# Kernel optimization log

Measured on AMD Instinct MI355X. Metric: run time of the kernel, lower is better.

## Reference

```python
import jax, jax.numpy as jnp
import numpy as np
from jax.scipy.special import logsumexp

UNK_ID = 1
B, T, V = 128, 33, 25000
E, H, D = 256, 256, 512
N, C = 8192, 16384
L = T - 1


def setup_inputs() -> dict:
    key = jax.random.key(0)
    ks = jax.random.split(key, 12)
    input_memories = jax.random.normal(ks[0], (N, D), jnp.float32)
    # each target owns a contiguous block of N//B memories (every segment non-empty)
    origin = jnp.repeat(jnp.arange(B, dtype=jnp.int32), N // B)
    initial_states = jax.random.normal(ks[1], (B, H), jnp.float32)
    target_token_ids = jax.random.randint(ks[2], (B, T), 0, V)
    # copyable elements: pick (memory n, time l); flat idx into [N,L] and [B,L]
    mem_pick = jax.random.randint(ks[3], (C,), 0, N)
    t_pick = jax.random.randint(ks[4], (C,), 0, L)
    copyable_elements_idxs = mem_pick * L + t_pick
    copyable_elements_sample_idxs = origin[mem_pick] * L + t_pick
    target_lengths = jax.random.randint(ks[5], (B,), 1, L + 1)
    emb_weight = 0.02 * jax.random.normal(ks[6], (V, E), jnp.float32)
    gru_w_ih = 0.05 * jax.random.normal(ks[7], (3 * H, E), jnp.float32)
    gru_w_hh = 0.05 * jax.random.normal(ks[8], (3 * H, H), jnp.float32)
    gru_b_ih = jnp.zeros((3 * H,), jnp.float32)
    gru_b_hh = jnp.zeros((3 * H,), jnp.float32)
    w_std_att = 0.05 * jax.random.normal(ks[9], (H, D), jnp.float32)
    w_copy_att = 0.05 * jax.random.normal(ks[10], (H, D), jnp.float32)
    hidden_to_vocab = 0.01 * jax.random.normal(ks[11], (2 * H, E), jnp.float32)
    vocab_bias = jnp.zeros((V,), jnp.float32)
    return dict(input_memories=input_memories, input_memories_origin_idx=origin,
                initial_states=initial_states, target_token_ids=target_token_ids,
                copyable_elements_idxs=copyable_elements_idxs,
                copyable_elements_sample_idxs=copyable_elements_sample_idxs,
                target_lengths=target_lengths, emb_weight=emb_weight,
                gru_w_ih=gru_w_ih, gru_w_hh=gru_w_hh, gru_b_ih=gru_b_ih,
                gru_b_hh=gru_b_hh, w_std_att=w_std_att, w_copy_att=w_copy_att,
                hidden_to_vocab=hidden_to_vocab, vocab_bias=vocab_bias)


def _gru(x, h0, w_ih, w_hh, b_ih, b_hh):
    # x: [B,L,E], h0: [B,H] -> outputs [B,L,H], last state [B,H]
    def step(h, xt):
        gi = xt @ w_ih.T + b_ih
        gh = h @ w_hh.T + b_hh
        ir, iz, inew = jnp.split(gi, 3, axis=-1)
        hr, hz, hnew = jnp.split(gh, 3, axis=-1)
        r = jax.nn.sigmoid(ir + hr)
        z = jax.nn.sigmoid(iz + hz)
        n = jnp.tanh(inew + r * hnew)
        h_next = (1.0 - z) * n + z * h
        return h_next, h_next
    h_last, ys = jax.lax.scan(step, h0, jnp.swapaxes(x, 0, 1))
    return jnp.swapaxes(ys, 0, 1), h_last


def _seg_log_softmax(x, idx, num_seg):
    m = jax.ops.segment_max(x, idx, num_segments=num_seg)
    x_sh = x - m[idx]
    s = jax.ops.segment_sum(jnp.exp(x_sh), idx, num_segments=num_seg)
    return x_sh - jnp.log(s)[idx]


def _seg_logsumexp(x, idx, num_seg):
    m = jax.ops.segment_max(x, idx, num_segments=num_seg)
    m_safe = jnp.where(jnp.isfinite(m), m, 0.0)
    s = jax.ops.segment_sum(jnp.exp(x - m_safe[idx]), idx, num_segments=num_seg)
    return jnp.where(s > 0, jnp.log(jnp.where(s > 0, s, 1.0)) + m_safe, -jnp.inf)


def reference(input_memories, input_memories_origin_idx, initial_states,
              target_token_ids, copyable_elements_idxs,
              copyable_elements_sample_idxs, target_lengths, emb_weight,
              gru_w_ih, gru_w_hh, gru_b_ih, gru_b_hh, w_std_att, w_copy_att,
              hidden_to_vocab, vocab_bias):
    origin = input_memories_origin_idx
    b, t = target_token_ids.shape
    l = t - 1
    tok_in = target_token_ids[:, :-1]
    tok_out = target_token_ids[:, 1:]

    x = emb_weight[tok_in]                                   # [B,L,E]
    out_states, _ = _gru(x, initial_states, gru_w_ih, gru_w_hh, gru_b_ih, gru_b_hh)
    std_reps = input_memories @ w_std_att.T                  # [N,H]
    copy_reps = input_memories @ w_copy_att.T                # [N,H]
    out_per_input = out_states[origin]                       # [N,L,H]
    std_scores = jnp.einsum('nlh,nh->nl', out_per_input, std_reps)
    copy_scores = jnp.einsum('nlh,nh->nl', out_per_input, copy_reps)

    std_logprobs = _seg_log_softmax(std_scores, origin, b)   # [N,L]
    std_mul = jnp.exp(std_logprobs)[:, :, None] * std_reps[:, None, :]
    std_out = jax.ops.segment_sum(std_mul, origin, num_segments=b)  # [B,L,H]

    cat = jnp.concatenate([std_out, out_states], axis=-1)    # [B,L,2H]
    target_scores = (cat @ hidden_to_vocab) @ emb_weight.T + vocab_bias  # [B,L,V]

    total_copy = _seg_logsumexp(copy_scores, origin, b)      # [B,L]
    all_scores = jnp.concatenate([target_scores, total_copy[:, :, None]], axis=-1)
    norm = logsumexp(all_scores, axis=-1)                    # [B,L]
    target_logprobs = target_scores - norm[:, :, None]
    copy_logprobs = copy_scores - norm[origin]               # [N,L]

    num_valid = jax.ops.segment_sum(jnp.ones_like(copyable_elements_sample_idxs),
                                    copyable_elements_sample_idxs,
                                    num_segments=b * l)
    valid_copy = num_valid.reshape(b, l) > 0
    unk_loc = tok_out == UNK_ID
    mask = valid_copy & unk_loc

    gen_lp = jnp.take_along_axis(target_logprobs, tok_out[:, :, None], axis=-1)[..., 0]
    gen_lp = jnp.where(mask, -jnp.inf, gen_lp)

    cc = _seg_logsumexp(copy_logprobs.reshape(-1)[copyable_elements_idxs],
                        copyable_elements_sample_idxs, b * l).reshape(b, l)

    any_lp = logsumexp(jnp.stack([gen_lp, cc]), axis=0)      # [B,L]
    len_mask = (jnp.arange(l)[None, :] < target_lengths[:, None]).astype(jnp.float32)
    per_seq = (any_lp * len_mask).sum(-1) / len_mask.sum(-1)
    return -per_seq.mean()
```

## Files before the change

### kernel.cpp

```cpp
#include <hip/hip_runtime.h>
#include <hip/hip_bf16.h>

#define UNK 1
constexpr int B  = 128, T = 33, V = 25000, E = 256, H = 256, D = 512;
constexpr int N  = 8192, C = 16384, L = 32;
constexpr int BL = B * L;
constexpr int VP = 25088;

typedef __attribute__((ext_vector_type(8))) short bf16x8;
typedef __attribute__((ext_vector_type(4))) float fx4;
typedef unsigned short u16;
typedef unsigned int u32;

__device__ __forceinline__ u16 f2b(float f) {
  u32 u = __float_as_uint(f);
  u += 0x7FFFu + ((u >> 16) & 1u);
  return (u16)(u >> 16);
}
__device__ __forceinline__ float b2f(u16 s) { return __uint_as_float(((u32)s) << 16); }
__device__ __forceinline__ float fsigm(float x) { return 1.f / (1.f + __expf(-x)); }
__device__ __forceinline__ float ftanh(float x) {
  float cx = fminf(fmaxf(x, -15.f), 15.f);
  float e = __expf(2.f * cx);
  return (e - 1.f) / (e + 1.f);
}
__device__ __forceinline__ u32 fkey(float f) {
  u32 b = __float_as_uint(f);
  return (b & 0x80000000u) ? ~b : (b | 0x80000000u);
}
__device__ __forceinline__ float fdec(u32 k) {
  u32 b = (k & 0x80000000u) ? (k & 0x7FFFFFFFu) : ~k;
  return __uint_as_float(b);
}
__device__ __forceinline__ void lcomb(float& M, float& S, float m2, float s2) {
  float Mn = fmaxf(M, m2);
  float a = (S  > 0.f) ? S  * expf(M  - Mn) : 0.f;
  float b = (s2 > 0.f) ? s2 * expf(m2 - Mn) : 0.f;
  M = Mn; S = a + b;
}
__device__ __forceinline__ void gload16(const void* g, void* l) {
  __builtin_amdgcn_global_load_lds(
      (const __attribute__((address_space(1))) void*)g,
      (__attribute__((address_space(3))) void*)l, 16, 0, 0);
}

constexpr int PB_EMB = VP * E / 1024;
constexpr int PB_MEM = N * D / 1024;
constexpr int PB_WIH = 768 * 256 / 1024;
constexpr int PB_WHH = 192;
constexpr int PB_WS  = 512 * 256 / 1024;
constexpr int PB_WC  = 128;
constexpr int PB_TR  = 512;
constexpr int PB_INIT= 16;
constexpr int PB_TOT = PB_EMB + PB_MEM + PB_WIH + PB_WHH + PB_WS + PB_WC + PB_TR + PB_INIT;

__device__ __forceinline__ void cvt4_at(const float* in, u16* out, int i) {
  float4 v = *(const float4*)&in[i];
  u16 r[4] = { f2b(v.x), f2b(v.y), f2b(v.z), f2b(v.w) };
  *(ushort4*)&out[i] = *(ushort4*)r;
}

__global__ void k_prep(const float* __restrict__ emb, const float* __restrict__ mem,
                       const float* __restrict__ wih, const float* __restrict__ whh,
                       const float* __restrict__ wstd, const float* __restrict__ wcpy,
                       const float* __restrict__ h2v,
                       u16* __restrict__ embb, u16* __restrict__ memb,
                       u16* __restrict__ wihb, u16* __restrict__ whb,
                       u16* __restrict__ wsb, u16* __restrict__ wcb,
                       u16* __restrict__ h2vtb,
                       u32* __restrict__ segk, float* __restrict__ segs,
                       int* __restrict__ nval, float* __restrict__ lacc) {
  int b = blockIdx.x, t = threadIdx.x;
  if (b < PB_EMB) {
    int i = (b * 256 + t) * 4;
    if (i + 3 < V * E) cvt4_at(emb, embb, i);
    else for (int j = 0; j < 4; ++j) embb[i + j] = (i + j < V * E) ? f2b(emb[i + j]) : (u16)0;
    return;
  }
  b -= PB_EMB;
  if (b < PB_MEM) { cvt4_at(mem, memb, (b * 256 + t) * 4); return; }
  b -= PB_MEM;
  if (b < PB_WIH) { cvt4_at(wih, wihb, (b * 256 + t) * 4); return; }
  b -= PB_WIH;
  if (b < PB_WHH) { cvt4_at(whh, whb, (b * 256 + t) * 4); return; }
  b -= PB_WHH;
  if (b < PB_WS)  { cvt4_at(wstd, wsb, (b * 256 + t) * 4); return; }
  b -= PB_WS;
  if (b < PB_WC)  { cvt4_at(wcpy, wcb, (b * 256 + t) * 4); return; }
  b -= PB_WC;
  if (b < PB_TR) {
    int f = b * 256 + t, j = f >> 9, k = f & 511;
    h2vtb[f] = f2b(h2v[k * 256 + j]);
    return;
  }
  b -= PB_TR;
  {
    int i = b * 256 + t;
    if (i < BL) { segk[i] = 0x007FFFFFu; segs[i] = 0.f; nval[i] = 0; }
    if (i == 0) lacc[0] = 0.f;
  }
}

__global__ __launch_bounds__(256, 2) void k_embgiM(const int* __restrict__ tok,
    const u16* __restrict__ eb, const u16* __restrict__ wih,
    const float* __restrict__ bih, const float* __restrict__ bhh,
    float* __restrict__ Git) {
  __shared__ __align__(16) u16 As[2][128 * 64];
  __shared__ __align__(16) u16 Bs2[2][128 * 64];
  int t = threadIdx.x;
  int m0 = blockIdx.x * 128, n0 = blockIdx.y * 128;
  int lane = t & 63, w = t >> 6, wm = w >> 1, wn = w & 1;
  int r16 = lane & 15, hi = lane >> 4;
  char* AsB = (char*)&As[0][0];
  char* BsB = (char*)&Bs2[0][0];
  int tk4[4];
#pragma unroll
  for (int i = 0; i < 4; ++i) {
    int row = (w * 4 + i) * 8 + (lane >> 3);
    int bl = m0 + row;
    tk4[i] = tok[(bl >> 5) * 33 + (bl & 31)];
  }
  fx4 acc[4][4] = {};
  auto stage = [&](int kt, int buf) {
#pragma unroll
    for (int i = 0; i < 4; ++i) {
      int s = (w * 4 + i) * 64 + lane;
      int row = s >> 3, sw = s & 7, c = sw ^ (row & 7);
      gload16(&eb[tk4[i] * 256 + kt * 64 + c * 8], AsB + buf * 16384 + (w * 4 + i) * 1024);
      gload16(&wih[(n0 + row) * 256 + kt * 64 + c * 8], BsB + buf * 16384 + (w * 4 + i) * 1024);
    }
  };
  stage(0, 0);
  for (int kt = 0; kt < 4; ++kt) {
    __syncthreads();
    if (kt < 3) stage(kt + 1, (kt + 1) & 1);
    int buf = kt & 1;
    bf16x8 afr[4][2], bfr[4][2];
#pragma unroll
    for (int mi = 0; mi < 4; ++mi)
#pragma unroll
      for (int kk = 0; kk < 2; ++kk) {
        int row = wm * 64 + mi * 16 + r16, cc = kk * 4 + hi;
        afr[mi][kk] = *(const bf16x8*)(AsB + buf * 16384 + (row * 8 + (cc ^ (row & 7))) * 16);
      }
#pragma unroll
    for (int ni = 0; ni < 4; ++ni)
#pragma unroll
      for (int kk = 0; kk < 2; ++kk) {
        int row = wn * 64 + ni * 16 + r16, cc = kk * 4 + hi;
        bfr[ni][kk] = *(const bf16x8*)(BsB + buf * 16384 + (row * 8 + (cc ^ (row & 7))) * 16);
      }
#pragma unroll
    for (int kk = 0; kk < 2; ++kk)
#pragma unroll
      for (int mi = 0; mi < 4; ++mi)
#pragma unroll
        for (int ni = 0; ni < 4; ++ni)
          acc[mi][ni] = __builtin_amdgcn_mfma_f32_16x16x32_bf16(afr[mi][kk], bfr[ni][kk], acc[mi][ni], 0, 0, 0);
  }
  float bihv[4];
#pragma unroll
  for (int ni = 0; ni < 4; ++ni) {
    int j = n0 + wn * 64 + ni * 16 + r16;
    bihv[ni] = bih[j] + (j < 512 ? bhh[j] : 0.f);
  }
#pragma unroll
  for (int mi = 0; mi < 4; ++mi)
#pragma unroll
    for (int ni = 0; ni < 4; ++ni)
#pragma unroll
      for (int q = 0; q < 4; ++q) {
        int bl = m0 + wm * 64 + mi * 16 + hi * 4 + q;
        int b = bl >> 5, st = bl & 31;
        int j  = n0 + wn * 64 + ni * 16 + r16;
        Git[(((b >> 4) * 32 + st) * 768 + j) * 16 + (b & 15)] = acc[mi][ni][q] + bihv[ni];
      }
}

__global__ __launch_bounds__(512, 2) void k_gru6(
    const float* __restrict__ Git, const u16* __restrict__ whb,
    const float* __restrict__ bhh, const float* __restrict__ h0,
    u16* __restrict__ outsb) {
  __shared__ u16 nfr[8 * 16 * 512];
  __shared__ u16 hbf[2][16 * 256];
  const int t = threadIdx.x;
  const int w = t >> 6, l = t & 63;
  const int lj = l & 15, lk = l >> 4;
  const int b0 = blockIdx.x * 16;

  bf16x8 fr[2][8], fz[2][8];
#pragma unroll
  for (int jh = 0; jh < 2; ++jh)
#pragma unroll
    for (int kc = 0; kc < 8; ++kc) {
      int jr = w * 32 + jh * 16 + lj;
      int k0 = kc * 32 + lk * 8;
      fr[jh][kc] = *(const bf16x8*)&whb[(0 * 256 + jr) * 256 + k0];
      fz[jh][kc] = *(const bf16x8*)&whb[(1 * 256 + jr) * 256 + k0];
      int4 nv = *(const int4*)&whb[(2 * 256 + jr) * 256 + k0];
      *(int4*)&nfr[((w * 16 + jh * 8 + kc) * 64 + l) * 8] = nv;
    }
#pragma unroll
  for (int jh = 0; jh < 2; ++jh)
#pragma unroll
    for (int kc = 0; kc < 8; ++kc) {
      asm volatile("" : "+v"(fr[jh][kc]));
      asm volatile("" : "+v"(fz[jh][kc]));
    }
  float bN[2];
#pragma unroll
  for (int jh = 0; jh < 2; ++jh) bN[jh] = bhh[512 + w * 32 + jh * 16 + lj];
  float hst[2][4];
#pragma unroll
  for (int jh = 0; jh < 2; ++jh)
#pragma unroll
    for (int q = 0; q < 4; ++q) {
      int m = lk * 4 + q, j = w * 32 + jh * 16 + lj;
      hst[jh][q] = h0[(b0 + m) * 256 + j];
      hbf[0][m * 256 + (((j >> 3) ^ (m & 7)) * 8) + (j & 7)] = f2b(hst[jh][q]);
    }
  __syncthreads();

  for (int st = 0; st < 32; ++st) {
    const float* gb = Git + (size_t)(blockIdx.x * 32 + st) * 768 * 16;
    fx4 grz[4];
#pragma unroll
    for (int g = 0; g < 2; ++g)
#pragma unroll
      for (int jh = 0; jh < 2; ++jh)
        grz[g * 2 + jh] = *(const fx4*)&gb[(g * 256 + w * 32 + jh * 16 + lj) * 16 + lk * 4];
    fx4 gn[2];
    fx4 accR[2] = {}, accZ[2] = {}, accN[2] = {};
    const u16* hb = hbf[st & 1];
#pragma unroll
    for (int kc = 0; kc < 8; ++kc) {
      int k8 = kc * 4 + lk;
      bf16x8 a = *(const bf16x8*)&hb[lj * 256 + ((k8 ^ (lj & 7)) * 8)];
      bf16x8 nf0 = *(const bf16x8*)&nfr[((w * 16 + 0 + kc) * 64 + l) * 8];
      bf16x8 nf1 = *(const bf16x8*)&nfr[((w * 16 + 8 + kc) * 64 + l) * 8];
      accR[0] = __builtin_amdgcn_mfma_f32_16x16x32_bf16(a, fr[0][kc], accR[0], 0, 0, 0);
      accR[1] = __builtin_amdgcn_mfma_f32_16x16x32_bf16(a, fr[1][kc], accR[1], 0, 0, 0);
      accZ[0] = __builtin_amdgcn_mfma_f32_16x16x32_bf16(a, fz[0][kc], accZ[0], 0, 0, 0);
      accZ[1] = __builtin_amdgcn_mfma_f32_16x16x32_bf16(a, fz[1][kc], accZ[1], 0, 0, 0);
      accN[0] = __builtin_amdgcn_mfma_f32_16x16x32_bf16(a, nf0, accN[0], 0, 0, 0);
      accN[1] = __builtin_amdgcn_mfma_f32_16x16x32_bf16(a, nf1, accN[1], 0, 0, 0);
      if (kc == 5) {
#pragma unroll
        for (int jh = 0; jh < 2; ++jh)
          gn[jh] = *(const fx4*)&gb[(2 * 256 + w * 32 + jh * 16 + lj) * 16 + lk * 4];
      }
    }
    u16* hw = (u16*)hbf[(st + 1) & 1];
#pragma unroll
    for (int jh = 0; jh < 2; ++jh)
#pragma unroll
      for (int q = 0; q < 4; ++q) {
        float r = fsigm(grz[jh][q] + accR[jh][q]);
        float z = fsigm(grz[2 + jh][q] + accZ[jh][q]);
        float n = ftanh(gn[jh][q] + r * (accN[jh][q] + bN[jh]));
        float hn = (1.f - z) * n + z * hst[jh][q];
        hst[jh][q] = hn;
        int m = lk * 4 + q, j = w * 32 + jh * 16 + lj;
        u16 hbv = f2b(hn);
        hw[m * 256 + (((j >> 3) ^ (m & 7)) * 8) + (j & 7)] = hbv;
        outsb[((size_t)(b0 + m) * 32 + st) * 256 + j] = hbv;
      }
    __syncthreads();
  }
}

__global__ __launch_bounds__(256, 2) void k_repsM(const u16* __restrict__ Am,
    const u16* __restrict__ wsb, const u16* __restrict__ wcb,
    float* __restrict__ sr, float* __restrict__ cr) {
  __shared__ __align__(16) u16 As[2][128 * 64];
  __shared__ __align__(16) u16 Bs2[2][128 * 64];
  int t = threadIdx.x;
  int m0 = blockIdx.x * 128, bn = blockIdx.y, n0 = bn * 128;
  const u16* Bsrc = (bn < 2) ? wsb : wcb;
  int jb = n0 & 255;
  int lane = t & 63, w = t >> 6, wm = w >> 1, wn = w & 1;
  int r16 = lane & 15, hi = lane >> 4;
  char* AsB = (char*)&As[0][0];
  char* BsB = (char*)&Bs2[0][0];
  fx4 acc[4][4] = {};
  auto stage = [&](int kt, int buf) {
#pragma unroll
    for (int i = 0; i < 4; ++i) {
      int s = (w * 4 + i) * 64 + lane;
      int row = s >> 3, sw = s & 7, c = sw ^ (row & 7);
      gload16(&Am[(m0 + row) * 512 + kt * 64 + c * 8], AsB + buf * 16384 + (w * 4 + i) * 1024);
      gload16(&Bsrc[(jb + row) * 512 + kt * 64 + c * 8], BsB + buf * 16384 + (w * 4 + i) * 1024);
    }
  };
  stage(0, 0);
  for (int kt = 0; kt < 8; ++kt) {
    __syncthreads();
    if (kt < 7) stage(kt + 1, (kt + 1) & 1);
    int buf = kt & 1;
    bf16x8 afr[4][2], bfr[4][2];
#pragma unroll
    for (int mi = 0; mi < 4; ++mi)
#pragma unroll
      for (int kk = 0; kk < 2; ++kk) {
        int row = wm * 64 + mi * 16 + r16, cc = kk * 4 + hi;
        afr[mi][kk] = *(const bf16x8*)(AsB + buf * 16384 + (row * 8 + (cc ^ (row & 7))) * 16);
      }
#pragma unroll
    for (int ni = 0; ni < 4; ++ni)
#pragma unroll
      for (int kk = 0; kk < 2; ++kk) {
        int row = wn * 64 + ni * 16 + r16, cc = kk * 4 + hi;
        bfr[ni][kk] = *(const bf16x8*)(BsB + buf * 16384 + (row * 8 + (cc ^ (row & 7))) * 16);
      }
#pragma unroll
    for (int kk = 0; kk < 2; ++kk)
#pragma unroll
      for (int mi = 0; mi < 4; ++mi)
#pragma unroll
        for (int ni = 0; ni < 4; ++ni)
          acc[mi][ni] = __builtin_amdgcn_mfma_f32_16x16x32_bf16(afr[mi][kk], bfr[ni][kk], acc[mi][ni], 0, 0, 0);
  }
#pragma unroll
  for (int mi = 0; mi < 4; ++mi)
#pragma unroll
    for (int ni = 0; ni < 4; ++ni)
#pragma unroll
      for (int q = 0; q < 4; ++q) {
        int mr = m0 + wm * 64 + mi * 16 + hi * 4 + q;
        int j  = n0 + wn * 64 + ni * 16 + r16;
        float vv = acc[mi][ni][q];
        if (j < 256) sr[mr * 256 + j] = vv; else cr[mr * 256 + (j - 256)] = vv;
      }
}

__global__ void k_scores(const u16* __restrict__ outsb, const float* __restrict__ sr,
                         const float* __restrict__ cr, float* __restrict__ ss,
                         float* __restrict__ cs) {
  __shared__ float os[32][257];
  int b = blockIdx.x >> 2, nc = blockIdx.x & 3, t = threadIdx.x;
  for (int i = 0; i < 8; ++i) {
    int q = t + 256 * i, row = q >> 6, c4 = q & 63;
    ushort4 v = *(const ushort4*)&outsb[(b * 32 + row) * 256 + c4 * 4];
    os[row][c4 * 4] = b2f(v.x); os[row][c4 * 4 + 1] = b2f(v.y);
    os[row][c4 * 4 + 2] = b2f(v.z); os[row][c4 * 4 + 3] = b2f(v.w);
  }
  __syncthreads();
  int l = t & 31, g = t >> 5;
  for (int rep = 0; rep < 2; ++rep) {
    int n = b * 64 + nc * 16 + g + rep * 8;
    float a = 0.f, c = 0.f;
    for (int k4 = 0; k4 < 64; ++k4) {
      float4 s4 = *(const float4*)&sr[n * 256 + k4 * 4];
      float4 c4v = *(const float4*)&cr[n * 256 + k4 * 4];
      float o0 = os[l][k4 * 4], o1 = os[l][k4 * 4 + 1];
      float o2 = os[l][k4 * 4 + 2], o3 = os[l][k4 * 4 + 3];
      a = fmaf(o0, s4.x, a); a = fmaf(o1, s4.y, a);
      a = fmaf(o2, s4.z, a); a = fmaf(o3, s4.w, a);
      c = fmaf(o0, c4v.x, c); c = fmaf(o1, c4v.y, c);
      c = fmaf(o2, c4v.z, c); c = fmaf(o3, c4v.w, c);
    }
    ss[n * 32 + l] = a; cs[n * 32 + l] = c;
  }
}

__global__ void k_smx(const float* __restrict__ ss, const float* __restrict__ cs,
                      const float* __restrict__ sr, u16* __restrict__ sob,
                      float* __restrict__ tc) {
  __shared__ float wst[64][33];
  __shared__ float wcp[64][33];
  int b = blockIdx.x, t = threadIdx.x;
  for (int i = 0; i < 8; ++i) {
    int q = t + 256 * i;
    wst[q >> 5][q & 31] = ss[b * 2048 + q];
    wcp[q >> 5][q & 31] = cs[b * 2048 + q];
  }
  __syncthreads();
  if (t < 32) {
    int l = t; float m = -1e30f;
    for (int n = 0; n < 64; ++n) m = fmaxf(m, wst[n][l]);
    float s = 0.f;
    for (int n = 0; n < 64; ++n) s += expf(wst[n][l] - m);
    float inv = 1.f / s;
    for (int n = 0; n < 64; ++n) wst[n][l] = expf(wst[n][l] - m) * inv;
  } else if (t < 64) {
    int l = t - 32; float m = -1e30f;
    for (int n = 0; n < 64; ++n) m = fmaxf(m, wcp[n][l]);
    float s = 0.f;
    for (int n = 0; n < 64; ++n) s += expf(wcp[n][l] - m);
    tc[b * 32 + l] = m + logf(s);
  }
  __syncthreads();
  float acc[32] = {};
  for (int n = 0; n < 64; ++n) {
    float v = sr[(b * 64 + n) * 256 + t];
#pragma unroll
    for (int l = 0; l < 32; ++l) acc[l] = fmaf(wst[n][l], v, acc[l]);
  }
  for (int l = 0; l < 32; ++l) sob[(b * 32 + l) * 256 + t] = f2b(acc[l]);
}

__global__ __launch_bounds__(256, 2) void k_projM(const u16* __restrict__ sob,
    const u16* __restrict__ outsb, const u16* __restrict__ h2vtb,
    u16* __restrict__ pb) {
  __shared__ __align__(16) u16 As[2][128 * 64];
  __shared__ __align__(16) u16 Bs2[2][128 * 64];
  int t = threadIdx.x;
  int m0 = blockIdx.x * 128, n0 = blockIdx.y * 128;
  int lane = t & 63, w = t >> 6, wm = w >> 1, wn = w & 1;
  int r16 = lane & 15, hi = lane >> 4;
  char* AsB = (char*)&As[0][0];
  char* BsB = (char*)&Bs2[0][0];
  fx4 acc[4][4] = {};
  auto stage = [&](int kt, int buf) {
    const u16* Asrc = (kt < 4) ? sob : outsb;
    int ko = (kt & 3) * 64;
#pragma unroll
    for (int i = 0; i < 4; ++i) {
      int s = (w * 4 + i) * 64 + lane;
      int row = s >> 3, sw = s & 7, c = sw ^ (row & 7);
      gload16(&Asrc[(m0 + row) * 256 + ko + c * 8], AsB + buf * 16384 + (w * 4 + i) * 1024);
      gload16(&h2vtb[(n0 + row) * 512 + kt * 64 + c * 8], BsB + buf * 16384 + (w * 4 + i) * 1024);
    }
  };
  stage(0, 0);
  for (int kt = 0; kt < 8; ++kt) {
    __syncthreads();
    if (kt < 7) stage(kt + 1, (kt + 1) & 1);
    int buf = kt & 1;
    bf16x8 afr[4][2], bfr[4][2];
#pragma unroll
    for (int mi = 0; mi < 4; ++mi)
#pragma unroll
      for (int kk = 0; kk < 2; ++kk) {
        int row = wm * 64 + mi * 16 + r16, cc = kk * 4 + hi;
        afr[mi][kk] = *(const bf16x8*)(AsB + buf * 16384 + (row * 8 + (cc ^ (row & 7))) * 16);
      }
#pragma unroll
    for (int ni = 0; ni < 4; ++ni)
#pragma unroll
      for (int kk = 0; kk < 2; ++kk) {
        int row = wn * 64 + ni * 16 + r16, cc = kk * 4 + hi;
        bfr[ni][kk] = *(const bf16x8*)(BsB + buf * 16384 + (row * 8 + (cc ^ (row & 7))) * 16);
      }
#pragma unroll
    for (int kk = 0; kk < 2; ++kk)
#pragma unroll
      for (int mi = 0; mi < 4; ++mi)
#pragma unroll
        for (int ni = 0; ni < 4; ++ni)
          acc[mi][ni] = __builtin_amdgcn_mfma_f32_16x16x32_bf16(afr[mi][kk], bfr[ni][kk], acc[mi][ni], 0, 0, 0);
  }
#pragma unroll
  for (int mi = 0; mi < 4; ++mi)
#pragma unroll
    for (int ni = 0; ni < 4; ++ni)
#pragma unroll
      for (int q = 0; q < 4; ++q) {
        int mr = m0 + wm * 64 + mi * 16 + hi * 4 + q;
        int j  = n0 + wn * 64 + ni * 16 + r16;
        pb[mr * 256 + j] = f2b(acc[mi][ni][q]);
      }
}

__global__ void k_gen(const u16* __restrict__ pb, const u16* __restrict__ eb,
                      const int* __restrict__ tok, const float* __restrict__ vb,
                      float* __restrict__ gs) {
  int w = threadIdx.x >> 6, lane = threadIdx.x & 63;
  int row = blockIdx.x * 4 + w;
  int b = row >> 5, l = row & 31;
  int tk = tok[b * 33 + l + 1];
  float s = 0.f;
#pragma unroll
  for (int i = 0; i < 4; ++i) {
    int k = lane * 4 + i;
    s += b2f(pb[row * 256 + k]) * b2f(eb[tk * 256 + k]);
  }
#pragma unroll
  for (int d = 1; d < 64; d <<= 1) s += __shfl_xor(s, d);
  if (lane == 0) gs[row] = s + vb[tk];
}

__global__ __launch_bounds__(256, 1) void k_gemm(const u16* __restrict__ A,
// ... 46 lines not shown
    fx4 acc[4][4] = {};
#pragma unroll
    for (int ks = 0; ks < 8; ++ks)
#pragma unroll
      for (int ni = 0; ni < 4; ++ni) {
        int row = wn * 64 + ni * 16 + r16;
        int g = ks * 4 + hi;
        int gp = (g & ~7) | ((g & 7) ^ (row & 7));
        bf16x8 bfv = *(const bf16x8*)(BsB + buf * 65536 + row * 512 + gp * 16);
#pragma unroll
        for (int mi = 0; mi < 4; ++mi)
          acc[mi][ni] = __builtin_amdgcn_mfma_f32_16x16x32_bf16(af[mi][ks], bfv, acc[mi][ni], 0, 0, 0);
      }
    float bias[4];
#pragma unroll
    for (int ni = 0; ni < 4; ++ni) {
      int v = cg * 128 + wn * 64 + ni * 16 + r16;
      bias[ni] = (v < V) ? vb[v] : -1e30f;
    }
#pragma unroll
    for (int mi = 0; mi < 4; ++mi)
#pragma unroll
      for (int q = 0; q < 4; ++q) {
        float e = 0.f;
#pragma unroll
        for (int ni = 0; ni < 4; ++ni)
          e += __expf(acc[mi][ni][q] + bias[ni]);
        Sa[mi][q] += e;
      }
  }
#undef STAGE

#pragma unroll
  for (int mi = 0; mi < 4; ++mi)
#pragma unroll
    for (int q = 0; q < 4; ++q) {
      float s = Sa[mi][q];
#pragma unroll
      for (int d = 1; d < 16; d <<= 1) s += __shfl_xor(s, d);
      Sa[mi][q] = s;
    }
  if (r16 == 0) {
#pragma unroll
    for (int mi = 0; mi < 4; ++mi)
#pragma unroll
      for (int q = 0; q < 4; ++q)
        red[wn][wm * 64 + mi * 16 + hi * 4 + q] = Sa[mi][q];
  }
  __syncthreads();
  if (t < 128)
    parts[(m0 + t) * 8 + vr] = red[0][t] + red[1][t];
}

__global__ void k_seg(const int* __restrict__ idx, const int* __restrict__ sid,
                      const float* __restrict__ cs, u32* __restrict__ sk,
                      int* __restrict__ nv) {
  int c = blockIdx.x * 256 + threadIdx.x;
  if (c < C) {
    int s = sid[c];
    atomicMax(&sk[s], fkey(cs[idx[c]]));
    atomicAdd(&nv[s], 1);
  }
}
__global__ void k_segsum(const int* __restrict__ idx, const int* __restrict__ sid,
                         const float* __restrict__ cs, const u32* __restrict__ sk,
                         float* __restrict__ ssum) {
  int c = blockIdx.x * 256 + threadIdx.x;
  if (c < C) {
    int s = sid[c];
    atomicAdd(&ssum[s], __expf(cs[idx[c]] - fdec(sk[s])));
  }
}

__global__ void k_final(const float* __restrict__ parts, const float* __restrict__ tc,
                        const float* __restrict__ gs, const u32* __restrict__ sk,
                        const float* __restrict__ ssum, const int* __restrict__ nv,
                        const int* __restrict__ tok, const int* __restrict__ tlen,
                        float* __restrict__ lacc) {
  int i = blockIdx.x * 256 + threadIdx.x;
  int b = i >> 5, l = i & 31;
  float S = 0.f;
#pragma unroll
  for (int r = 0; r < 8; ++r) S += parts[i * 8 + r];
  float M = 0.f, Ss = S;
  lcomb(M, Ss, tc[i], 1.f);
  float nrm = M + logf(Ss);
  int tk = tok[b * 33 + l + 1];
  float glp = gs[i] - nrm;
  int cnt = nv[i];
  if (cnt > 0 && tk == UNK) glp = -INFINITY;
  float cc = (cnt > 0) ? (logf(ssum[i]) + fdec(sk[i]) - nrm) : -INFINITY;
  float m = fmaxf(glp, cc);
  float any = (m == -INFINITY) ? -INFINITY : m + logf(expf(glp - m) + expf(cc - m));
  float oa = (l < tlen[b]) ? any : 0.f;
#pragma unroll
  for (int d = 1; d < 32; d <<= 1) oa += __shfl_xor(oa, d);
  if (l == 0) atomicAdd(lacc, oa / (float)tlen[b]);
}

__global__ void k_loss(const float* __restrict__ lacc, float* __restrict__ out) {
  out[0] = -lacc[0] / 128.f;
}

extern "C" void kernel_launch(void* const* d_in, const int* in_sizes, int n_in,
                              void* d_out, int out_size, void* d_ws, size_t ws_size,
                              hipStream_t stream) {
  const float* mem  = (const float*)d_in[0];
  const float* h0   = (const float*)d_in[2];
  const int*   tok  = (const int*)d_in[3];
  const int*   cidx = (const int*)d_in[4];
  const int*   csid = (const int*)d_in[5];
  const int*   tlen = (const int*)d_in[6];
  const float* emb  = (const float*)d_in[7];
  const float* wih  = (const float*)d_in[8];
  const float* whh  = (const float*)d_in[9];
  const float* bih  = (const float*)d_in[10];
  const float* bhh  = (const float*)d_in[11];
  const float* wstd = (const float*)d_in[12];
  const float* wcpy = (const float*)d_in[13];
  const float* h2v  = (const float*)d_in[14];
  const float* vb   = (const float*)d_in[15];

  char* ws = (char*)d_ws;
  size_t off = 0;
  auto alloc = [&](size_t bytes) -> char* {
    char* p = ws + off;
    off = (off + bytes + 255) & ~(size_t)255;
    return p;
  };
  u16*    embb  = (u16*)   alloc((size_t)VP * E * 2);
  u16*    memb  = (u16*)   alloc((size_t)N * D * 2);
  u16*    wihb  = (u16*)   alloc(768 * 256 * 2);
  u16*    whb   = (u16*)   alloc(768 * 256 * 2);
  u16*    wsb   = (u16*)   alloc(256 * 512 * 2);
  u16*    wcb   = (u16*)   alloc(256 * 512 * 2);
  u16*    h2vtb = (u16*)   alloc(256 * 512 * 2);
  float*  Git   = (float*) alloc((size_t)BL * 768 * 4);
  u16*    outsb = (u16*)   alloc((size_t)BL * 256 * 2);
  u16*    stdob = (u16*)   alloc((size_t)BL * 256 * 2);
  float*  sreps = (float*) alloc((size_t)N * 256 * 4);
  float*  creps = (float*) alloc((size_t)N * 256 * 4);
  float*  sscr  = (float*) alloc((size_t)N * 32 * 4);
  float*  cscr  = (float*) alloc((size_t)N * 32 * 4);
  float*  tcopy = (float*) alloc(BL * 4);
  u16*    projb = (u16*)   alloc((size_t)BL * 256 * 2);
  float*  parts = (float*) alloc((size_t)BL * 8 * 4);
  float*  gens  = (float*) alloc(BL * 4);
  u32*    segk  = (u32*)   alloc(BL * 4);
  float*  segs  = (float*) alloc(BL * 4);
  int*    nval  = (int*)   alloc(BL * 4);
  float*  lacc  = (float*) alloc(256);
  (void)ws_size; (void)in_sizes; (void)n_in; (void)out_size;

  k_prep<<<PB_TOT, 256, 0, stream>>>(emb, mem, wih, whh, wstd, wcpy, h2v,
                                     embb, memb, wihb, whb, wsb, wcb, h2vtb,
                                     segk, segs, nval, lacc);
  k_embgiM<<<dim3(32, 6), 256, 0, stream>>>(tok, embb, wihb, bih, bhh, Git);
  k_gru6<<<8, 512, 0, stream>>>(Git, whb, bhh, h0, outsb);
  k_repsM<<<dim3(64, 4), 256, 0, stream>>>(memb, wsb, wcb, sreps, creps);
  k_scores<<<512, 256, 0, stream>>>(outsb, sreps, creps, sscr, cscr);
  k_seg<<<64, 256, 0, stream>>>(cidx, csid, cscr, segk, nval);
  k_segsum<<<64, 256, 0, stream>>>(cidx, csid, cscr, segk, segs);
  k_smx<<<128, 256, 0, stream>>>(sscr, cscr, sreps, stdob, tcopy);
  k_projM<<<dim3(32, 2), 256, 0, stream>>>(stdob, outsb, h2vtb, projb);
  k_gen<<<1024, 256, 0, stream>>>(projb, embb, tok, vb, gens);
  k_gemm<<<256, 256, 0, stream>>>(projb, embb, vb, parts);
  k_final<<<16, 256, 0, stream>>>(parts, tcopy, gens, segk, segs, nval, tok, tlen, lacc);
  k_loss<<<1, 1, 0, stream>>>(lacc, (float*)d_out);
}
```

Before: 287.2 us.

## Split GRU recurrence across 16 blocks of 8 batch rows with 4 waves

The GRU recurrent kernel now processes 8 batch rows per block instead of 16, launching 16 blocks of 256 threads instead of 8 blocks of 512. Each wave covers 64 hidden units with 4 fragments, holding twice as many recurrent weight fragments in registers. The precomputed input-gate buffer layout changes to match, with 8 batch rows interleaved per group instead of 16. The aim is to spread the serial 32-step recurrence over more CUs so each step finishes sooner. In exchange, half of each 16-row MFMA tile is wasted on duplicated rows, and register pressure per thread rises.

```diff
diff --git a/kernel.cpp b/kernel.cpp
--- a/kernel.cpp
+++ b/kernel.cpp
@@ -173,97 +173,101 @@
         int bl = m0 + wm * 64 + mi * 16 + hi * 4 + q;
         int b = bl >> 5, st = bl & 31;
         int j  = n0 + wn * 64 + ni * 16 + r16;
-        Git[(((b >> 4) * 32 + st) * 768 + j) * 16 + (b & 15)] = acc[mi][ni][q] + bihv[ni];
-      }
-}
-
-__global__ __launch_bounds__(512, 2) void k_gru6(
+        Git[(((size_t)(b >> 3) * 32 + st) * 768 + j) * 8 + (b & 7)] = acc[mi][ni][q] + bihv[ni];
+      }
+}
+
+__global__ __launch_bounds__(256, 1) void k_gru7(
     const float* __restrict__ Git, const u16* __restrict__ whb,
     const float* __restrict__ bhh, const float* __restrict__ h0,
     u16* __restrict__ outsb) {
-  __shared__ u16 nfr[8 * 16 * 512];
-  __shared__ u16 hbf[2][16 * 256];
+  __shared__ u16 nfr[4 * 32 * 512];
+  __shared__ u16 hbf[2][8 * 256];
   const int t = threadIdx.x;
   const int w = t >> 6, l = t & 63;
   const int lj = l & 15, lk = l >> 4;
-  const int b0 = blockIdx.x * 16;
-
-  bf16x8 fr[2][8], fz[2][8];
-#pragma unroll
-  for (int jh = 0; jh < 2; ++jh)
+  const int lkc = lk & 1;
+  const int b0 = blockIdx.x * 8;
+
+  bf16x8 fr[4][8], fz[4][8];
+#pragma unroll
+  for (int jf = 0; jf < 4; ++jf)
 #pragma unroll
     for (int kc = 0; kc < 8; ++kc) {
-      int jr = w * 32 + jh * 16 + lj;
+      int jr = w * 64 + jf * 16 + lj;
       int k0 = kc * 32 + lk * 8;
-      fr[jh][kc] = *(const bf16x8*)&whb[(0 * 256 + jr) * 256 + k0];
-      fz[jh][kc] = *(const bf16x8*)&whb[(1 * 256 + jr) * 256 + k0];
+      fr[jf][kc] = *(const bf16x8*)&whb[(0 * 256 + jr) * 256 + k0];
+      fz[jf][kc] = *(const bf16x8*)&whb[(1 * 256 + jr) * 256 + k0];
       int4 nv = *(const int4*)&whb[(2 * 256 + jr) * 256 + k0];
-      *(int4*)&nfr[((w * 16 + jh * 8 + kc) * 64 + l) * 8] = nv;
-    }
-#pragma unroll
-  for (int jh = 0; jh < 2; ++jh)
+      *(int4*)&nfr[((w * 32 + jf * 8 + kc) * 64 + l) * 8] = nv;
+    }
+#pragma unroll
+  for (int jf = 0; jf < 4; ++jf)
 #pragma unroll
     for (int kc = 0; kc < 8; ++kc) {
-      asm volatile("" : "+v"(fr[jh][kc]));
-      asm volatile("" : "+v"(fz[jh][kc]));
-    }
-  float bN[2];
-#pragma unroll
-  for (int jh = 0; jh < 2; ++jh) bN[jh] = bhh[512 + w * 32 + jh * 16 + lj];
-  float hst[2][4];
-#pragma unroll
-  for (int jh = 0; jh < 2; ++jh)
+      asm volatile("" : "+v"(fr[jf][kc]));
+      asm volatile("" : "+v"(fz[jf][kc]));
+    }
+  float bN[4];
+#pragma unroll
+  for (int jf = 0; jf < 4; ++jf) bN[jf] = bhh[512 + w * 64 + jf * 16 + lj];
+  float hst[4][4];
+#pragma unroll
+  for (int jf = 0; jf < 4; ++jf)
 #pragma unroll
     for (int q = 0; q < 4; ++q) {
-      int m = lk * 4 + q, j = w * 32 + jh * 16 + lj;
-      hst[jh][q] = h0[(b0 + m) * 256 + j];
-      hbf[0][m * 256 + (((j >> 3) ^ (m & 7)) * 8) + (j & 7)] = f2b(hst[jh][q]);
+      int m = lkc * 4 + q, j = w * 64 + jf * 16 + lj;
+      hst[jf][q] = h0[(b0 + m) * 256 + j];
+      if (lk < 2)
+        hbf[0][m * 256 + (((j >> 3) ^ m) * 8) + (j & 7)] = f2b(hst[jf][q]);
     }
   __syncthreads();
 
   for (int st = 0; st < 32; ++st) {
-    const float* gb = Git + (size_t)(blockIdx.x * 32 + st) * 768 * 16;
-    fx4 grz[4];
+    const float* gb = Git + (size_t)(blockIdx.x * 32 + st) * 768 * 8;
+    fx4 grz[2][4];
 #pragma unroll
     for (int g = 0; g < 2; ++g)
 #pragma unroll
-      for (int jh = 0; jh < 2; ++jh)
-        grz[g * 2 + jh] = *(const fx4*)&gb[(g * 256 + w * 32 + jh * 16 + lj) * 16 + lk * 4];
-    fx4 gn[2];
-    fx4 accR[2] = {}, accZ[2] = {}, accN[2] = {};
+      for (int jf = 0; jf < 4; ++jf)
+        grz[g][jf] = *(const fx4*)&gb[(g * 256 + w * 64 + jf * 16 + lj) * 8 + lkc * 4];
+    fx4 gn[4];
+    fx4 accR[4] = {}, accZ[4] = {}, accN[4] = {};
     const u16* hb = hbf[st & 1];
+    const int ar = l & 7;
 #pragma unroll
     for (int kc = 0; kc < 8; ++kc) {
       int k8 = kc * 4 + lk;
-      bf16x8 a = *(const bf16x8*)&hb[lj * 256 + ((k8 ^ (lj & 7)) * 8)];
-      bf16x8 nf0 = *(const bf16x8*)&nfr[((w * 16 + 0 + kc) * 64 + l) * 8];
-      bf16x8 nf1 = *(const bf16x8*)&nfr[((w * 16 + 8 + kc) * 64 + l) * 8];
-      accR[0] = __builtin_amdgcn_mfma_f32_16x16x32_bf16(a, fr[0][kc], accR[0], 0, 0, 0);
-      accR[1] = __builtin_amdgcn_mfma_f32_16x16x32_bf16(a, fr[1][kc], accR[1], 0, 0, 0);
-      accZ[0] = __builtin_amdgcn_mfma_f32_16x16x32_bf16(a, fz[0][kc], accZ[0], 0, 0, 0);
-      accZ[1] = __builtin_amdgcn_mfma_f32_16x16x32_bf16(a, fz[1][kc], accZ[1], 0, 0, 0);
-      accN[0] = __builtin_amdgcn_mfma_f32_16x16x32_bf16(a, nf0, accN[0], 0, 0, 0);
-      accN[1] = __builtin_amdgcn_mfma_f32_16x16x32_bf16(a, nf1, accN[1], 0, 0, 0);
+      bf16x8 a = *(const bf16x8*)&hb[ar * 256 + ((k8 ^ ar) * 8)];
+#pragma unroll
+      for (int jf = 0; jf < 4; ++jf) {
+        bf16x8 nf = *(const bf16x8*)&nfr[((w * 32 + jf * 8 + kc) * 64 + l) * 8];
+        accR[jf] = __builtin_amdgcn_mfma_f32_16x16x32_bf16(a, fr[jf][kc], accR[jf], 0, 0, 0);
+        accZ[jf] = __builtin_amdgcn_mfma_f32_16x16x32_bf16(a, fz[jf][kc], accZ[jf], 0, 0, 0);
+        accN[jf] = __builtin_amdgcn_mfma_f32_16x16x32_bf16(a, nf, accN[jf], 0, 0, 0);
+      }
       if (kc == 5) {
 #pragma unroll
-        for (int jh = 0; jh < 2; ++jh)
-          gn[jh] = *(const fx4*)&gb[(2 * 256 + w * 32 + jh * 16 + lj) * 16 + lk * 4];
+        for (int jf = 0; jf < 4; ++jf)
+          gn[jf] = *(const fx4*)&gb[(2 * 256 + w * 64 + jf * 16 + lj) * 8 + lkc * 4];
       }
     }
     u16* hw = (u16*)hbf[(st + 1) & 1];
 #pragma unroll
-    for (int jh = 0; jh < 2; ++jh)
+    for (int jf = 0; jf < 4; ++jf)
 #pragma unroll
       for (int q = 0; q < 4; ++q) {
-        float r = fsigm(grz[jh][q] + accR[jh][q]);
-        float z = fsigm(grz[2 + jh][q] + accZ[jh][q]);
-        float n = ftanh(gn[jh][q] + r * (accN[jh][q] + bN[jh]));
-        float hn = (1.f - z) * n + z * hst[jh][q];
-        hst[jh][q] = hn;
-        int m = lk * 4 + q, j = w * 32 + jh * 16 + lj;
-        u16 hbv = f2b(hn);
-        hw[m * 256 + (((j >> 3) ^ (m & 7)) * 8) + (j & 7)] = hbv;
-        outsb[((size_t)(b0 + m) * 32 + st) * 256 + j] = hbv;
+        float r = fsigm(grz[0][jf][q] + accR[jf][q]);
+        float z = fsigm(grz[1][jf][q] + accZ[jf][q]);
+        float n = ftanh(gn[jf][q] + r * (accN[jf][q] + bN[jf]));
+        float hn = (1.f - z) * n + z * hst[jf][q];
+        hst[jf][q] = hn;
+        if (lk < 2) {
+          int m = lkc * 4 + q, j = w * 64 + jf * 16 + lj;
+          u16 hbv = f2b(hn);
+          hw[m * 256 + (((j >> 3) ^ m) * 8) + (j & 7)] = hbv;
+          outsb[((size_t)(b0 + m) * 32 + st) * 256 + j] = hbv;
+        }
       }
     __syncthreads();
   }
@@ -684,7 +688,7 @@
                                      embb, memb, wihb, whb, wsb, wcb, h2vtb,
                                      segk, segs, nval, lacc);
   k_embgiM<<<dim3(32, 6), 256, 0, stream>>>(tok, embb, wihb, bih, bhh, Git);
-  k_gru6<<<8, 512, 0, stream>>>(Git, whb, bhh, h0, outsb);
+  k_gru7<<<16, 256, 0, stream>>>(Git, whb, bhh, h0, outsb);
   k_repsM<<<dim3(64, 4), 256, 0, stream>>>(memb, wsb, wcb, sreps, creps);
   k_scores<<<512, 256, 0, stream>>>(outsb, sreps, creps, sscr, cscr);
   k_seg<<<64, 256, 0, stream>>>(cidx, csid, cscr, segk, nval);
```

New measurement: 342.7 us. 19.3% more time.

## Co-schedule GRU recurrence with memory-reps GEMM and fold prep into input-gate GEMM

Applied to the files above, without the earlier changes.

Splits the conversion kernel so only the embedding and W_ih casts run before the input-gate GEMM. The remaining casts and initialisation now run as extra blocks inside that GEMM launch. The 8-block sequential GRU kernel is merged with the memory representation GEMM into one 136-block launch, so the reps GEMM fills otherwise idle CUs while the recurrence runs. The reps blocks use 8 waves with a shared A tile across two 128-column groups. This adds shared-memory pressure (144KB per block) and removes the register-pinning asm barriers in the GRU path, which could change register allocation.

```diff
diff --git a/kernel.cpp b/kernel.cpp
--- a/kernel.cpp
+++ b/kernel.cpp
@@ -44,71 +44,74 @@
       (__attribute__((address_space(3))) void*)l, 16, 0, 0);
 }
 
-constexpr int PB_EMB = VP * E / 1024;
-constexpr int PB_MEM = N * D / 1024;
-constexpr int PB_WIH = 768 * 256 / 1024;
-constexpr int PB_WHH = 192;
-constexpr int PB_WS  = 512 * 256 / 1024;
-constexpr int PB_WC  = 128;
-constexpr int PB_TR  = 512;
-constexpr int PB_INIT= 16;
-constexpr int PB_TOT = PB_EMB + PB_MEM + PB_WIH + PB_WHH + PB_WS + PB_WC + PB_TR + PB_INIT;
-
 __device__ __forceinline__ void cvt4_at(const float* in, u16* out, int i) {
   float4 v = *(const float4*)&in[i];
   u16 r[4] = { f2b(v.x), f2b(v.y), f2b(v.z), f2b(v.w) };
   *(ushort4*)&out[i] = *(ushort4*)r;
 }
 
-__global__ void k_prep(const float* __restrict__ emb, const float* __restrict__ mem,
-                       const float* __restrict__ wih, const float* __restrict__ whh,
-                       const float* __restrict__ wstd, const float* __restrict__ wcpy,
-                       const float* __restrict__ h2v,
-                       u16* __restrict__ embb, u16* __restrict__ memb,
-                       u16* __restrict__ wihb, u16* __restrict__ whb,
-                       u16* __restrict__ wsb, u16* __restrict__ wcb,
-                       u16* __restrict__ h2vtb,
-                       u32* __restrict__ segk, float* __restrict__ segs,
-                       int* __restrict__ nval, float* __restrict__ lacc) {
+constexpr int PA_EMB = VP * E / 1024;
+constexpr int PA_WIH = 768 * 256 / 1024;
+constexpr int PA_TOT = PA_EMB + PA_WIH;
+
+__global__ void k_prepA(const float* __restrict__ emb, const float* __restrict__ wih,
+                        u16* __restrict__ embb, u16* __restrict__ wihb) {
   int b = blockIdx.x, t = threadIdx.x;
-  if (b < PB_EMB) {
+  if (b < PA_EMB) {
     int i = (b * 256 + t) * 4;
     if (i + 3 < V * E) cvt4_at(emb, embb, i);
     else for (int j = 0; j < 4; ++j) embb[i + j] = (i + j < V * E) ? f2b(emb[i + j]) : (u16)0;
     return;
   }
-  b -= PB_EMB;
-  if (b < PB_MEM) { cvt4_at(mem, memb, (b * 256 + t) * 4); return; }
-  b -= PB_MEM;
-  if (b < PB_WIH) { cvt4_at(wih, wihb, (b * 256 + t) * 4); return; }
-  b -= PB_WIH;
-  if (b < PB_WHH) { cvt4_at(whh, whb, (b * 256 + t) * 4); return; }
-  b -= PB_WHH;
-  if (b < PB_WS)  { cvt4_at(wstd, wsb, (b * 256 + t) * 4); return; }
-  b -= PB_WS;
-  if (b < PB_WC)  { cvt4_at(wcpy, wcb, (b * 256 + t) * 4); return; }
-  b -= PB_WC;
-  if (b < PB_TR) {
-    int f = b * 256 + t, j = f >> 9, k = f & 511;
-    h2vtb[f] = f2b(h2v[k * 256 + j]);
-    return;
-  }
-  b -= PB_TR;
-  {
+  b -= PA_EMB;
+  cvt4_at(wih, wihb, (b * 256 + t) * 4);
+}
+
+constexpr int EB_GI  = 192;
+constexpr int PBB_MEM = N * D / 1024;
+constexpr int PBB_WHH = 192;
+constexpr int PBB_WS  = 128;
+constexpr int PBB_WC  = 128;
+constexpr int PBB_TR  = 512;
+constexpr int PBB_INIT= 16;
+constexpr int EB_TOT = EB_GI + PBB_MEM + PBB_WHH + PBB_WS + PBB_WC + PBB_TR + PBB_INIT;
+
+__global__ __launch_bounds__(256, 2) void k_embgiB(const int* __restrict__ tok,
+    const u16* __restrict__ eb, const u16* __restrict__ wih,
+    const float* __restrict__ bih, const float* __restrict__ bhh,
+    float* __restrict__ Git,
+    const float* __restrict__ mem, const float* __restrict__ whh,
+    const float* __restrict__ wstd, const float* __restrict__ wcpy,
+    const float* __restrict__ h2v,
+    u16* __restrict__ memb, u16* __restrict__ whb,
+    u16* __restrict__ wsb, u16* __restrict__ wcb, u16* __restrict__ h2vtb,
+    u32* __restrict__ segk, float* __restrict__ segs,
+    int* __restrict__ nval, float* __restrict__ lacc) {
+  __shared__ __align__(16) u16 As[2][128 * 64];
+  __shared__ __align__(16) u16 Bs2[2][128 * 64];
+  int e = blockIdx.x, t = threadIdx.x;
+  if (e >= EB_GI) {
+    int b = e - EB_GI;
+    if (b < PBB_MEM) { cvt4_at(mem, memb, (b * 256 + t) * 4); return; }
+    b -= PBB_MEM;
+    if (b < PBB_WHH) { cvt4_at(whh, whb, (b * 256 + t) * 4); return; }
+    b -= PBB_WHH;
+    if (b < PBB_WS)  { cvt4_at(wstd, wsb, (b * 256 + t) * 4); return; }
+    b -= PBB_WS;
+    if (b < PBB_WC)  { cvt4_at(wcpy, wcb, (b * 256 + t) * 4); return; }
+    b -= PBB_WC;
+    if (b < PBB_TR) {
+      int f = b * 256 + t, j = f >> 9, k = f & 511;
+      h2vtb[f] = f2b(h2v[k * 256 + j]);
+      return;
+    }
+    b -= PBB_TR;
     int i = b * 256 + t;
     if (i < BL) { segk[i] = 0x007FFFFFu; segs[i] = 0.f; nval[i] = 0; }
     if (i == 0) lacc[0] = 0.f;
-  }
-}
-
-__global__ __launch_bounds__(256, 2) void k_embgiM(const int* __restrict__ tok,
-    const u16* __restrict__ eb, const u16* __restrict__ wih,
-    const float* __restrict__ bih, const float* __restrict__ bhh,
-    float* __restrict__ Git) {
-  __shared__ __align__(16) u16 As[2][128 * 64];
-  __shared__ __align__(16) u16 Bs2[2][128 * 64];
-  int t = threadIdx.x;
-  int m0 = blockIdx.x * 128, n0 = blockIdx.y * 128;
+    return;
+  }
+  int m0 = (e & 31) * 128, n0 = (e >> 5) * 128;
   int lane = t & 63, w = t >> 6, wm = w >> 1, wn = w & 1;
   int r16 = lane & 15, hi = lane >> 4;
   char* AsB = (char*)&As[0][0];
@@ -173,123 +176,127 @@
         int bl = m0 + wm * 64 + mi * 16 + hi * 4 + q;
         int b = bl >> 5, st = bl & 31;
         int j  = n0 + wn * 64 + ni * 16 + r16;
-        Git[(((b >> 4) * 32 + st) * 768 + j) * 16 + (b & 15)] = acc[mi][ni][q] + bihv[ni];
-      }
-}
-
-__global__ __launch_bounds__(512, 2) void k_gru6(
+        Git[(((size_t)(b >> 4) * 32 + st) * 768 + j) * 16 + (b & 15)] = acc[mi][ni][q] + bihv[ni];
+      }
+}
+
+__global__ __launch_bounds__(512, 2) void k_grureps(
     const float* __restrict__ Git, const u16* __restrict__ whb,
     const float* __restrict__ bhh, const float* __restrict__ h0,
-    u16* __restrict__ outsb) {
-  __shared__ u16 nfr[8 * 16 * 512];
-  __shared__ u16 hbf[2][16 * 256];
+    u16* __restrict__ outsb,
+    const u16* __restrict__ Am, const u16* __restrict__ wsb,
+    const u16* __restrict__ wcb, float* __restrict__ sr, float* __restrict__ cr) {
+  __shared__ __align__(16) char smem[147456];
   const int t = threadIdx.x;
   const int w = t >> 6, l = t & 63;
-  const int lj = l & 15, lk = l >> 4;
-  const int b0 = blockIdx.x * 16;
-
-  bf16x8 fr[2][8], fz[2][8];
-#pragma unroll
-  for (int jh = 0; jh < 2; ++jh)
-#pragma unroll
-    for (int kc = 0; kc < 8; ++kc) {
-      int jr = w * 32 + jh * 16 + lj;
-      int k0 = kc * 32 + lk * 8;
-      fr[jh][kc] = *(const bf16x8*)&whb[(0 * 256 + jr) * 256 + k0];
-      fz[jh][kc] = *(const bf16x8*)&whb[(1 * 256 + jr) * 256 + k0];
-      int4 nv = *(const int4*)&whb[(2 * 256 + jr) * 256 + k0];
-      *(int4*)&nfr[((w * 16 + jh * 8 + kc) * 64 + l) * 8] = nv;
+
+  if (blockIdx.x < 8) {
+    u16* nfr = (u16*)smem;
+    u16* hbf0 = (u16*)(smem + 131072);
+    u16* hbf1 = (u16*)(smem + 131072 + 8192);
+    const int lj = l & 15, lk = l >> 4;
+    const int b0 = blockIdx.x * 16;
+
+    bf16x8 fr[2][8], fz[2][8];
+#pragma unroll
+    for (int jh = 0; jh < 2; ++jh)
+#pragma unroll
+      for (int kc = 0; kc < 8; ++kc) {
+        int jr = w * 32 + jh * 16 + lj;
+        int k0 = kc * 32 + lk * 8;
+        fr[jh][kc] = *(const bf16x8*)&whb[(0 * 256 + jr) * 256 + k0];
+        fz[jh][kc] = *(const bf16x8*)&whb[(1 * 256 + jr) * 256 + k0];
+        int4 nv = *(const int4*)&whb[(2 * 256 + jr) * 256 + k0];
+        *(int4*)&nfr[((w * 16 + jh * 8 + kc) * 64 + l) * 8] = nv;
+      }
+    float bN[2];
+#pragma unroll
+    for (int jh = 0; jh < 2; ++jh) bN[jh] = bhh[512 + w * 32 + jh * 16 + lj];
+    float hst[2][4];
+#pragma unroll
+    for (int jh = 0; jh < 2; ++jh)
+#pragma unroll
+      for (int q = 0; q < 4; ++q) {
+        int m = lk * 4 + q, j = w * 32 + jh * 16 + lj;
+        hst[jh][q] = h0[(b0 + m) * 256 + j];
+        hbf0[m * 256 + (((j >> 3) ^ (m & 7)) * 8) + (j & 7)] = f2b(hst[jh][q]);
+      }
+    __syncthreads();
+
+    for (int st = 0; st < 32; ++st) {
+      const float* gb = Git + (size_t)(blockIdx.x * 32 + st) * 768 * 16;
+      fx4 grz[4];
+#pragma unroll
+      for (int g = 0; g < 2; ++g)
+#pragma unroll
+        for (int jh = 0; jh < 2; ++jh)
+          grz[g * 2 + jh] = *(const fx4*)&gb[(g * 256 + w * 32 + jh * 16 + lj) * 16 + lk * 4];
+      fx4 gn[2];
+      fx4 accR[2] = {}, accZ[2] = {}, accN[2] = {};
+      const u16* hb = (st & 1) ? hbf1 : hbf0;
+#pragma unroll
+      for (int kc = 0; kc < 8; ++kc) {
+        int k8 = kc * 4 + lk;
+        bf16x8 a = *(const bf16x8*)&hb[lj * 256 + ((k8 ^ (lj & 7)) * 8)];
+        bf16x8 nf0 = *(const bf16x8*)&nfr[((w * 16 + 0 + kc) * 64 + l) * 8];
+        bf16x8 nf1 = *(const bf16x8*)&nfr[((w * 16 + 8 + kc) * 64 + l) * 8];
+        accR[0] = __builtin_amdgcn_mfma_f32_16x16x32_bf16(a, fr[0][kc], accR[0], 0, 0, 0);
+        accR[1] = __builtin_amdgcn_mfma_f32_16x16x32_bf16(a, fr[1][kc], accR[1], 0, 0, 0);
+        accZ[0] = __builtin_amdgcn_mfma_f32_16x16x32_bf16(a, fz[0][kc], accZ[0], 0, 0, 0);
+        accZ[1] = __builtin_amdgcn_mfma_f32_16x16x32_bf16(a, fz[1][kc], accZ[1], 0, 0, 0);
+        accN[0] = __builtin_amdgcn_mfma_f32_16x16x32_bf16(a, nf0, accN[0], 0, 0, 0);
+        accN[1] = __builtin_amdgcn_mfma_f32_16x16x32_bf16(a, nf1, accN[1], 0, 0, 0);
+        if (kc == 5) {
+#pragma unroll
+          for (int jh = 0; jh < 2; ++jh)
+            gn[jh] = *(const fx4*)&gb[(2 * 256 + w * 32 + jh * 16 + lj) * 16 + lk * 4];
+        }
+      }
+      u16* hw = (st & 1) ? hbf0 : hbf1;
+#pragma unroll
+      for (int jh = 0; jh < 2; ++jh)
+#pragma unroll
+        for (int q = 0; q < 4; ++q) {
+          float r = fsigm(grz[jh][q] + accR[jh][q]);
+          float z = fsigm(grz[2 + jh][q] + accZ[jh][q]);
+          float n = ftanh(gn[jh][q] + r * (accN[jh][q] + bN[jh]));
+          float hn = (1.f - z) * n + z * hst[jh][q];
+          hst[jh][q] = hn;
+          int m = lk * 4 + q, j = w * 32 + jh * 16 + lj;
+          u16 hbv = f2b(hn);
+          hw[m * 256 + (((j >> 3) ^ (m & 7)) * 8) + (j & 7)] = hbv;
+          outsb[((size_t)(b0 + m) * 32 + st) * 256 + j] = hbv;
+        }
+      __syncthreads();
     }
-#pragma unroll
-  for (int jh = 0; jh < 2; ++jh)
-#pragma unroll
-    for (int kc = 0; kc < 8; ++kc) {
-      asm volatile("" : "+v"(fr[jh][kc]));
-      asm volatile("" : "+v"(fz[jh][kc]));
-    }
-  float bN[2];
-#pragma unroll
-  for (int jh = 0; jh < 2; ++jh) bN[jh] = bhh[512 + w * 32 + jh * 16 + lj];
-  float hst[2][4];
-#pragma unroll
-  for (int jh = 0; jh < 2; ++jh)
-#pragma unroll
-    for (int q = 0; q < 4; ++q) {
-      int m = lk * 4 + q, j = w * 32 + jh * 16 + lj;
-      hst[jh][q] = h0[(b0 + m) * 256 + j];
-      hbf[0][m * 256 + (((j >> 3) ^ (m & 7)) * 8) + (j & 7)] = f2b(hst[jh][q]);
-    }
-  __syncthreads();
-
-  for (int st = 0; st < 32; ++st) {
-    const float* gb = Git + (size_t)(blockIdx.x * 32 + st) * 768 * 16;
-    fx4 grz[4];
-#pragma unroll
-    for (int g = 0; g < 2; ++g)
-#pragma unroll
-      for (int jh = 0; jh < 2; ++jh)
-        grz[g * 2 + jh] = *(const fx4*)&gb[(g * 256 + w * 32 + jh * 16 + lj) * 16 + lk * 4];
-    fx4 gn[2];
-    fx4 accR[2] = {}, accZ[2] = {}, accN[2] = {};
-    const u16* hb = hbf[st & 1];
-#pragma unroll
-    for (int kc = 0; kc < 8; ++kc) {
-      int k8 = kc * 4 + lk;
-      bf16x8 a = *(const bf16x8*)&hb[lj * 256 + ((k8 ^ (lj & 7)) * 8)];
-      bf16x8 nf0 = *(const bf16x8*)&nfr[((w * 16 + 0 + kc) * 64 + l) * 8];
-      bf16x8 nf1 = *(const bf16x8*)&nfr[((w * 16 + 8 + kc) * 64 + l) * 8];
-      accR[0] = __builtin_amdgcn_mfma_f32_16x16x32_bf16(a, fr[0][kc], accR[0], 0, 0, 0);
-      accR[1] = __builtin_amdgcn_mfma_f32_16x16x32_bf16(a, fr[1][kc], accR[1], 0, 0, 0);
-      accZ[0] = __builtin_amdgcn_mfma_f32_16x16x32_bf16(a, fz[0][kc], accZ[0], 0, 0, 0);
-      accZ[1] = __builtin_amdgcn_mfma_f32_16x16x32_bf16(a, fz[1][kc], accZ[1], 0, 0, 0);
-      accN[0] = __builtin_amdgcn_mfma_f32_16x16x32_bf16(a, nf0, accN[0], 0, 0, 0);
-      accN[1] = __builtin_amdgcn_mfma_f32_16x16x32_bf16(a, nf1, accN[1], 0, 0, 0);
-      if (kc == 5) {
-#pragma unroll
-        for (int jh = 0; jh < 2; ++jh)
-          gn[jh] = *(const fx4*)&gb[(2 * 256 + w * 32 + jh * 16 + lj) * 16 + lk * 4];
-      }
-    }
-    u16* hw = (u16*)hbf[(st + 1) & 1];
-#pragma unroll
-    for (int jh = 0; jh < 2; ++jh)
-#pragma unroll
-      for (int q = 0; q < 4; ++q) {
-        float r = fsigm(grz[jh][q] + accR[jh][q]);
-        float z = fsigm(grz[2 + jh][q] + accZ[jh][q]);
-        float n = ftanh(gn[jh][q] + r * (accN[jh][q] + bN[jh]));
-        float hn = (1.f - z) * n + z * hst[jh][q];
-        hst[jh][q] = hn;
-        int m = lk * 4 + q, j = w * 32 + jh * 16 + lj;
-        u16 hbv = f2b(hn);
-        hw[m * 256 + (((j >> 3) ^ (m & 7)) * 8) + (j & 7)] = hbv;
-        outsb[((size_t)(b0 + m) * 32 + st) * 256 + j] = hbv;
-      }
-    __syncthreads();
-  }
-}
-
-__global__ __launch_bounds__(256, 2) void k_repsM(const u16* __restrict__ Am,
-    const u16* __restrict__ wsb, const u16* __restrict__ wcb,
-    float* __restrict__ sr, float* __restrict__ cr) {
-  __shared__ __align__(16) u16 As[2][128 * 64];
-  __shared__ __align__(16) u16 Bs2[2][128 * 64];
-  int t = threadIdx.x;
-  int m0 = blockIdx.x * 128, bn = blockIdx.y, n0 = bn * 128;
-  const u16* Bsrc = (bn < 2) ? wsb : wcb;
-  int jb = n0 & 255;
-  int lane = t & 63, w = t >> 6, wm = w >> 1, wn = w & 1;
-  int r16 = lane & 15, hi = lane >> 4;
-  char* AsB = (char*)&As[0][0];
-  char* BsB = (char*)&Bs2[0][0];
+    return;
+  }
+
+  int rb = blockIdx.x - 8;
+  int m0 = (rb >> 1) * 128, sn = rb & 1;
+  const u16* Bsrc = sn ? wcb : wsb;
+  int grp = w >> 2, wg = w & 3, wm = wg >> 1, wn = wg & 1;
+  int jb = grp * 128;
+  int lane = l, r16 = lane & 15, hi = lane >> 4;
+  char* AsB = smem;
+  char* BsB = smem + 32768 + grp * 32768;
   fx4 acc[4][4] = {};
   auto stage = [&](int kt, int buf) {
-#pragma unroll
-    for (int i = 0; i < 4; ++i) {
-      int s = (w * 4 + i) * 64 + lane;
-      int row = s >> 3, sw = s & 7, c = sw ^ (row & 7);
-      gload16(&Am[(m0 + row) * 512 + kt * 64 + c * 8], AsB + buf * 16384 + (w * 4 + i) * 1024);
-      gload16(&Bsrc[(jb + row) * 512 + kt * 64 + c * 8], BsB + buf * 16384 + (w * 4 + i) * 1024);
+    if (grp == 0) {
+#pragma unroll
+      for (int i = 0; i < 4; ++i) {
+        int s = (wg * 4 + i) * 64 + lane;
+        int row = s >> 3, sw = s & 7, c = sw ^ (row & 7);
+        gload16(&Am[(m0 + row) * 512 + kt * 64 + c * 8], AsB + buf * 16384 + (wg * 4 + i) * 1024);
+        gload16(&Bsrc[(0 + row) * 512 + kt * 64 + c * 8], (smem + 32768) + buf * 16384 + (wg * 4 + i) * 1024);
+      }
+    } else {
+#pragma unroll
+      for (int i = 0; i < 4; ++i) {
+        int s = (wg * 4 + i) * 64 + lane;
+        int row = s >> 3, sw = s & 7, c = sw ^ (row & 7);
+        gload16(&Bsrc[(128 + row) * 512 + kt * 64 + c * 8], (smem + 65536) + buf * 16384 + (wg * 4 + i) * 1024);
+      }
     }
   };
   stage(0, 0);
@@ -327,7 +334,7 @@
 #pragma unroll
       for (int q = 0; q < 4; ++q) {
         int mr = m0 + wm * 64 + mi * 16 + hi * 4 + q;
-        int j  = n0 + wn * 64 + ni * 16 + r16;
+        int j  = sn * 256 + jb + wn * 64 + ni * 16 + r16;
         float vv = acc[mi][ni][q];
         if (j < 256) sr[mr * 256 + j] = vv; else cr[mr * 256 + (j - 256)] = vv;
       }
@@ -680,12 +687,13 @@
   float*  lacc  = (float*) alloc(256);
   (void)ws_size; (void)in_sizes; (void)n_in; (void)out_size;
 
-  k_prep<<<PB_TOT, 256, 0, stream>>>(emb, mem, wih, whh, wstd, wcpy, h2v,
-                                     embb, memb, wihb, whb, wsb, wcb, h2vtb,
-                                     segk, segs, nval, lacc);
-  k_embgiM<<<dim3(32, 6), 256, 0, stream>>>(tok, embb, wihb, bih, bhh, Git);
-  k_gru6<<<8, 512, 0, stream>>>(Git, whb, bhh, h0, outsb);
-  k_repsM<<<dim3(64, 4), 256, 0, stream>>>(memb, wsb, wcb, sreps, creps);
+  k_prepA<<<PA_TOT, 256, 0, stream>>>(emb, wih, embb, wihb);
+  k_embgiB<<<EB_TOT, 256, 0, stream>>>(tok, embb, wihb, bih, bhh, Git,
+                                       mem, whh, wstd, wcpy, h2v,
+                                       memb, whb, wsb, wcb, h2vtb,
+                                       segk, segs, nval, lacc);
+  k_grureps<<<136, 512, 0, stream>>>(Git, whb, bhh, h0, outsb,
+                                     memb, wsb, wcb, sreps, creps);
   k_scores<<<512, 256, 0, stream>>>(outsb, sreps, creps, sscr, cscr);
   k_seg<<<64, 256, 0, stream>>>(cidx, csid, cscr, segk, nval);
   k_segsum<<<64, 256, 0, stream>>>(cidx, csid, cscr, segk, segs);
```

After: 284.8 us. About the same (-0.8%).
